# Kernel optimization log

Measured on AMD Instinct MI355X. Metric: run time of the kernel, lower is better.

Reference implementation:

```python
import jax, jax.numpy as jnp
import numpy as np

N_NODES = 50000
IN_CH = 128
HID = 128
OUT_CH = 40
N_LAYERS = 3
N_EDGES = 600000


def setup_inputs() -> dict:
    key = jax.random.key(0)
    ks = jax.random.split(key, 4 + 5 * N_LAYERS)
    x = jax.random.normal(ks[0], (N_NODES, IN_CH), dtype=jnp.float32)
    edge_attr = jax.random.normal(ks[1], (N_EDGES, 4), dtype=jnp.float32)
    edge_index = jax.random.randint(ks[2], (2, N_EDGES), 0, N_NODES, dtype=jnp.int64)
    # Per-layer MLP params ([in->hid->hid]); in==hid so stack as [L, d, d].
    def glorot(k, fan_in, fan_out):
        s = jnp.sqrt(2.0 / (fan_in + fan_out)).astype(jnp.float32)
        return jax.random.normal(k, (fan_in, fan_out), dtype=jnp.float32) * s
    W1 = jnp.stack([glorot(ks[3 + i], IN_CH if i == 0 else HID, HID) for i in range(N_LAYERS)])
    b1 = jnp.zeros((N_LAYERS, HID), dtype=jnp.float32)
    W2 = jnp.stack([glorot(ks[3 + N_LAYERS + i], HID, HID) for i in range(N_LAYERS)])
    b2 = jnp.zeros((N_LAYERS, HID), dtype=jnp.float32)
    Wc = glorot(ks[3 + 2 * N_LAYERS], HID, OUT_CH)
    bc = jnp.zeros((OUT_CH,), dtype=jnp.float32)
    return {"x": x, "edge_attr": edge_attr, "edge_index": edge_index,
            "W1": W1, "b1": b1, "W2": W2, "b2": b2, "Wc": Wc, "bc": bc}


def reference(x, edge_attr, edge_index, W1, b1, W2, b2, Wc, bc):
    # GIN node classifier, eval mode (dropout = identity, BN = identity).
    src, dst = edge_index[0], edge_index[1]
    h = x
    for i in range(N_LAYERS):
        # GINConv (eps=0): aggregate sum of neighbor features via scatter-add.
        msgs = h[src]                                   # [E, d] gather
        aggr = jax.ops.segment_sum(msgs, dst, num_segments=N_NODES)  # [N, d]
        z = h + aggr                                    # (1+eps)*x + sum
        z = jax.nn.relu(z @ W1[i] + b1[i])              # MLP hidden
        z = z @ W2[i] + b2[i]                           # MLP out
        h = jax.nn.relu(z)                              # F.relu(conv(...))
    return h @ Wc + bc                                  # [N, OUT_CH]
```

## Files before the change

### kernel.cpp

```cpp
#include <hip/hip_runtime.h>

#define N_NODES 50000
#define IN_CH 128
#define HID 128
#define OUT_CH 40
#define N_LAYERS 3
#define N_EDGES 600000
#define DSTRIDE 64
#define DEGSTRIDE 32

typedef __attribute__((ext_vector_type(8))) short short8;
typedef __attribute__((ext_vector_type(4))) float floatx4;

static __device__ __forceinline__ unsigned short f32_to_bf16(float f) {
  unsigned u = __float_as_uint(f);
  unsigned r = 0x7FFFu + ((u >> 16) & 1u);
  return (unsigned short)((u + r) >> 16);
}
static __device__ __forceinline__ float bf16_to_f32(unsigned short h) {
  return __uint_as_float(((unsigned)h) << 16);
}

#define CONV_BLOCKS 6250
#define W_BLOCKS 408
#define DEG_BLOCKS 1563

__global__ __launch_bounds__(256) void prep_all_kernel(
    const float* __restrict__ x, const float* __restrict__ W1,
    const float* __restrict__ W2, const float* __restrict__ Wc,
    unsigned short* __restrict__ xb, unsigned short* __restrict__ WT,
    unsigned short* __restrict__ WcT, unsigned short* __restrict__ hb1,
    int* __restrict__ deg) {
  const int b = blockIdx.x;
  const int t = threadIdx.x;
  if (b < CONV_BLOCKS) {
    int i = (b * 256 + t) * 4;
    if (i < N_NODES * 128) {
      float4 v = *(const float4*)(x + i);
      ushort4 o;
      o.x = f32_to_bf16(v.x); o.y = f32_to_bf16(v.y);
      o.z = f32_to_bf16(v.z); o.w = f32_to_bf16(v.w);
      *(ushort4*)(xb + i) = o;
    }
  } else if (b < CONV_BLOCKS + W_BLOCKS) {
    int o = (b - CONV_BLOCKS) * 256 + t;
    if (o < 6 * 16384) {
      int mat = o >> 14;
      int r = o & 16383;
      int n = r >> 7;
      int k = r & 127;
      const float* W = (mat < 3) ? (W1 + (size_t)mat * 16384)
                                 : (W2 + (size_t)(mat - 3) * 16384);
      WT[(size_t)mat * 16384 + (size_t)n * 128 + k] =
          f32_to_bf16(W[(size_t)k * 128 + n]);
    } else if (o < 6 * 16384 + 48 * 128) {
      int r = o - 6 * 16384;
      int n = r >> 7;
      int k = r & 127;
      float v = (n < OUT_CH) ? Wc[(size_t)k * OUT_CH + n] : 0.0f;
      WcT[(size_t)n * 128 + k] = f32_to_bf16(v);
    }
  } else if (b < CONV_BLOCKS + W_BLOCKS + DEG_BLOCKS) {
    int i = ((b - CONV_BLOCKS - W_BLOCKS) * 256 + t) * 4;
    if (i < N_NODES * DEGSTRIDE) *(int4*)(deg + i) = make_int4(0, 0, 0, 0);
  } else {
    if (t < 128) xb[(size_t)N_NODES * 128 + t] = 0;
    else hb1[(size_t)N_NODES * 128 + (t - 128)] = 0;
  }
}

#define CSR_BLOCKS 586
__global__ __launch_bounds__(256) void csr_kernel(
    const int* __restrict__ ei, int* __restrict__ deg, int* __restrict__ col) {
  int base = (blockIdx.x * 256 + threadIdx.x) * 4;
  if (base >= N_EDGES) return;
  int4 s4 = *(const int4*)(ei + base);
  int4 d4 = *(const int4*)(ei + N_EDGES + base);
  int p0 = atomicAdd(&deg[(size_t)d4.x * DEGSTRIDE], 1);
  int p1 = atomicAdd(&deg[(size_t)d4.y * DEGSTRIDE], 1);
  int p2 = atomicAdd(&deg[(size_t)d4.z * DEGSTRIDE], 1);
  int p3 = atomicAdd(&deg[(size_t)d4.w * DEGSTRIDE], 1);
  col[(size_t)d4.x * DSTRIDE + p0] = s4.x;
  col[(size_t)d4.y * DSTRIDE + p1] = s4.y;
  col[(size_t)d4.z * DSTRIDE + p2] = s4.z;
  col[(size_t)d4.w * DSTRIDE + p3] = s4.w;
}

__global__ __launch_bounds__(256) void aggregate_kernel(
    const unsigned short* __restrict__ h, const int* __restrict__ deg,
    const int* __restrict__ col, unsigned short* __restrict__ z) {
  int n = __builtin_amdgcn_readfirstlane(blockIdx.x * 4 + (threadIdx.x >> 6));
  int q = threadIdx.x & 63;
  const size_t co = (size_t)q * 2;
  ushort2 sv = *(const ushort2*)(h + (size_t)n * 128 + co);
  float ax[8], ay[8];
#pragma unroll
  for (int k = 0; k < 8; ++k) { ax[k] = 0.f; ay[k] = 0.f; }
  ax[0] = bf16_to_f32(sv.x);
  ay[0] = bf16_to_f32(sv.y);
  int dg = __builtin_amdgcn_readfirstlane(deg[(size_t)n * DEGSTRIDE]);
  int cnt = (dg + 15) & ~15;
  const int* cp = col + (size_t)n * DSTRIDE;
  for (int i = 0; i < cnt; i += 16) {
    int ss[16];
#pragma unroll
    for (int k = 0; k < 16; ++k) {
      int sl = cp[i + k];
      ss[k] = __builtin_amdgcn_readfirstlane((i + k < dg) ? sl : N_NODES);
    }
    ushort2 vv[16];
#pragma unroll
    for (int k = 0; k < 16; ++k)
      vv[k] = *(const ushort2*)(h + (size_t)ss[k] * 128 + co);
#pragma unroll
    for (int k = 0; k < 16; ++k) {
      ax[k & 7] += bf16_to_f32(vv[k].x);
      ay[k & 7] += bf16_to_f32(vv[k].y);
    }
  }
  float s0 = (ax[0] + ax[1]) + (ax[2] + ax[3]) + (ax[4] + ax[5]) + (ax[6] + ax[7]);
  float s1 = (ay[0] + ay[1]) + (ay[2] + ay[3]) + (ay[4] + ay[5]) + (ay[6] + ay[7]);
  ushort2 o;
  o.x = f32_to_bf16(s0);
  o.y = f32_to_bf16(s1);
  *(ushort2*)(z + (size_t)n * 128 + co) = o;
}

template <bool LAST>
__global__ __launch_bounds__(256) void layer_pair_kernel(
    const unsigned short* __restrict__ A, const unsigned short* __restrict__ WT1,
    const float* __restrict__ b1, const unsigned short* __restrict__ WT2,
    const float* __restrict__ b2, unsigned short* __restrict__ Z,
    const unsigned short* __restrict__ WcT, const float* __restrict__ bc,
    float* __restrict__ out, int M) {
  __shared__ __align__(16) unsigned short Wl[128][136];
  __shared__ __align__(16) unsigned short T[64][136];
  const int tid = threadIdx.x;
  const int w = tid >> 6;
  const int lane = tid & 63;
  const int qg = lane >> 4;
  const int ln = lane & 15;
  const int row0 = blockIdx.x * 64;
  const int rbase = w * 16;
  const int r0 = row0 + rbase + ln;
  const short8 zero8 = {0, 0, 0, 0, 0, 0, 0, 0};

#pragma unroll
  for (int j = 0; j < 8; ++j) {
    int slot = tid + j * 256;
    int row = slot >> 4;
    int kb = slot & 15;
    *(short8*)&Wl[row][kb * 8] = *(const short8*)(WT1 + (size_t)row * 128 + kb * 8);
  }
  __syncthreads();

  floatx4 acc[8];
#pragma unroll
  for (int ct = 0; ct < 8; ++ct) acc[ct] = (floatx4){0.f, 0.f, 0.f, 0.f};
#pragma unroll
  for (int ks = 0; ks < 4; ++ks) {
    const int koff = ks * 32 + qg * 8;
    short8 a = (r0 < M) ? *(const short8*)(A + (size_t)r0 * 128 + koff) : zero8;
#pragma unroll
    for (int ct = 0; ct < 8; ++ct) {
      short8 b = *(const short8*)&Wl[ct * 16 + ln][koff];
      acc[ct] = __builtin_amdgcn_mfma_f32_16x16x32_bf16(a, b, acc[ct], 0, 0, 0);
    }
  }
#pragma unroll
  for (int ct = 0; ct < 8; ++ct) {
    float bv = b1[ct * 16 + ln];
#pragma unroll
    for (int r = 0; r < 4; ++r) {
      float v = fmaxf(acc[ct][r] + bv, 0.0f);
      T[rbase + qg * 4 + r][ct * 16 + ln] = f32_to_bf16(v);
    }
  }

  __syncthreads();
#pragma unroll
  for (int j = 0; j < 8; ++j) {
    int slot = tid + j * 256;
    int row = slot >> 4;
    int kb = slot & 15;
    *(short8*)&Wl[row][kb * 8] = *(const short8*)(WT2 + (size_t)row * 128 + kb * 8);
  }
  __syncthreads();

  floatx4 acc2[8];
#pragma unroll
  for (int ct = 0; ct < 8; ++ct) acc2[ct] = (floatx4){0.f, 0.f, 0.f, 0.f};
#pragma unroll
  for (int ks = 0; ks < 4; ++ks) {
    const int koff = ks * 32 + qg * 8;
    short8 a = *(const short8*)&T[rbase + ln][koff];
#pragma unroll
    for (int ct = 0; ct < 8; ++ct) {
      short8 b = *(const short8*)&Wl[ct * 16 + ln][koff];
      acc2[ct] = __builtin_amdgcn_mfma_f32_16x16x32_bf16(a, b, acc2[ct], 0, 0, 0);
    }
  }
#pragma unroll
  for (int ct = 0; ct < 8; ++ct) {
    float bv = b2[ct * 16 + ln];
#pragma unroll
    for (int r = 0; r < 4; ++r) {
      float v = fmaxf(acc2[ct][r] + bv, 0.0f);
      T[rbase + qg * 4 + r][ct * 16 + ln] = f32_to_bf16(v);
    }
  }

  if (LAST) {
    floatx4 acc3[3];
#pragma unroll
    for (int ct = 0; ct < 3; ++ct) acc3[ct] = (floatx4){0.f, 0.f, 0.f, 0.f};
#pragma unroll
    for (int ks = 0; ks < 4; ++ks) {
      const int koff = ks * 32 + qg * 8;
      short8 a = *(const short8*)&T[rbase + ln][koff];
#pragma unroll
      for (int ct = 0; ct < 3; ++ct) {
        short8 b = *(const short8*)(WcT + (size_t)(ct * 16 + ln) * 128 + koff);
        acc3[ct] = __builtin_amdgcn_mfma_f32_16x16x32_bf16(a, b, acc3[ct], 0, 0, 0);
      }
    }
#pragma unroll
    for (int ct = 0; ct < 3; ++ct) {
      int colg = ct * 16 + ln;
      if (colg < OUT_CH) {
        float bv = bc[colg];
#pragma unroll
        for (int r = 0; r < 4; ++r) {
          int row = row0 + rbase + qg * 4 + r;
          if (row < M) out[(size_t)row * OUT_CH + colg] = acc3[ct][r] + bv;
        }
      }
    }
  } else {
    __syncthreads();
#pragma unroll
    for (int j = 0; j < 4; ++j) {
      int slot = tid + j * 256;
      int row = slot >> 4;
      int kb = slot & 15;
      if (row0 + row < M) {
        short8 v = *(const short8*)&T[row][kb * 8];
        *(short8*)(Z + (size_t)(row0 + row) * 128 + kb * 8) = v;
      }
    }
  }
}

extern "C" void kernel_launch(void* const* d_in, const int* in_sizes, int n_in,
                              void* d_out, int out_size, void* d_ws,
                              size_t ws_size, hipStream_t stream) {
  const float* x = (const float*)d_in[0];
  const int* ei = (const int*)d_in[2];
  const float* W1 = (const float*)d_in[3];
  const float* b1 = (const float*)d_in[4];
  const float* W2 = (const float*)d_in[5];
  const float* b2 = (const float*)d_in[6];
  const float* Wc = (const float*)d_in[7];
  const float* bc = (const float*)d_in[8];
  float* out = (float*)d_out;

  const size_t NF = (size_t)(N_NODES + 1) * 128;
  unsigned short* hb0 = (unsigned short*)d_ws;
  unsigned short* hb1 = hb0 + NF;
  unsigned short* xbf = hb1 + NF;
  unsigned short* WT = xbf + NF;
  unsigned short* WcT = WT + 6 * 16384;
  int* deg = (int*)(WcT + 48 * 128);
  int* col = deg + (size_t)N_NODES * DEGSTRIDE;

  const dim3 blk(256);
  const int aggr_grid = N_NODES / 4;
  const int pair_grid = (N_NODES + 63) / 64;

  prep_all_kernel<<<CONV_BLOCKS + W_BLOCKS + DEG_BLOCKS + 1, blk, 0, stream>>>(
      x, W1, W2, Wc, xbf, WT, WcT, hb1, deg);

  csr_kernel<<<CSR_BLOCKS, blk, 0, stream>>>(ei, deg, col);

  const unsigned short* h = xbf;
  for (int l = 0; l < N_LAYERS; ++l) {
    aggregate_kernel<<<aggr_grid, blk, 0, stream>>>(h, deg, col, hb0);
    if (l < N_LAYERS - 1) {
      layer_pair_kernel<false><<<pair_grid, blk, 0, stream>>>(
          hb0, WT + (size_t)l * 16384, b1 + (size_t)l * 128,
          WT + (size_t)(3 + l) * 16384, b2 + (size_t)l * 128, hb1,
          nullptr, nullptr, nullptr, N_NODES);
      h = hb1;
    } else {
      layer_pair_kernel<true><<<pair_grid, blk, 0, stream>>>(
          hb0, WT + (size_t)l * 16384, b1 + (size_t)l * 128,
          WT + (size_t)(3 + l) * 16384, b2 + (size_t)l * 128, nullptr,
          WcT, bc, out, N_NODES);
    }
  }
}
```

Measured before the change: 245.5 us.

## Overlap CSR build with bf16 conversion by moving deg zeroing to its own kernel

Measured after the change: 243.2 us. Within noise of the previous version (-0.9%).

```diff
diff --git a/kernel.cpp b/kernel.cpp
--- a/kernel.cpp
+++ b/kernel.cpp
@@ -7,7 +7,7 @@
 #define N_LAYERS 3
 #define N_EDGES 600000
 #define DSTRIDE 64
-#define DEGSTRIDE 32
+#define DEGSTRIDE 16
 
 typedef __attribute__((ext_vector_type(8))) short short8;
 typedef __attribute__((ext_vector_type(4))) float floatx4;
@@ -21,20 +21,41 @@
   return __uint_as_float(((unsigned)h) << 16);
 }
 
+#define ZERO_BLOCKS 782
+__global__ __launch_bounds__(256) void zero_deg_kernel(int* __restrict__ deg) {
+  int i = (blockIdx.x * 256 + threadIdx.x) * 4;
+  if (i < N_NODES * DEGSTRIDE) *(int4*)(deg + i) = make_int4(0, 0, 0, 0);
+}
+
+#define CSRB 586
 #define CONV_BLOCKS 6250
 #define W_BLOCKS 408
-#define DEG_BLOCKS 1563
-
-__global__ __launch_bounds__(256) void prep_all_kernel(
+
+__global__ __launch_bounds__(256) void prep_csr_kernel(
     const float* __restrict__ x, const float* __restrict__ W1,
     const float* __restrict__ W2, const float* __restrict__ Wc,
-    unsigned short* __restrict__ xb, unsigned short* __restrict__ WT,
-    unsigned short* __restrict__ WcT, unsigned short* __restrict__ hb1,
-    int* __restrict__ deg) {
+    const int* __restrict__ ei, unsigned short* __restrict__ xb,
+    unsigned short* __restrict__ WT, unsigned short* __restrict__ WcT,
+    unsigned short* __restrict__ hb1, int* __restrict__ deg,
+    int* __restrict__ col) {
   const int b = blockIdx.x;
   const int t = threadIdx.x;
-  if (b < CONV_BLOCKS) {
-    int i = (b * 256 + t) * 4;
+  if (b < CSRB) {
+    int base = (b * 256 + t) * 4;
+    if (base < N_EDGES) {
+      int4 s4 = *(const int4*)(ei + base);
+      int4 d4 = *(const int4*)(ei + N_EDGES + base);
+      int p0 = atomicAdd(&deg[(size_t)d4.x * DEGSTRIDE], 1);
+      int p1 = atomicAdd(&deg[(size_t)d4.y * DEGSTRIDE], 1);
+      int p2 = atomicAdd(&deg[(size_t)d4.z * DEGSTRIDE], 1);
+      int p3 = atomicAdd(&deg[(size_t)d4.w * DEGSTRIDE], 1);
+      col[(size_t)d4.x * DSTRIDE + p0] = s4.x;
+      col[(size_t)d4.y * DSTRIDE + p1] = s4.y;
+      col[(size_t)d4.z * DSTRIDE + p2] = s4.z;
+      col[(size_t)d4.w * DSTRIDE + p3] = s4.w;
+    }
+  } else if (b < CSRB + CONV_BLOCKS) {
+    int i = ((b - CSRB) * 256 + t) * 4;
     if (i < N_NODES * 128) {
       float4 v = *(const float4*)(x + i);
       ushort4 o;
@@ -42,8 +63,8 @@
       o.z = f32_to_bf16(v.z); o.w = f32_to_bf16(v.w);
       *(ushort4*)(xb + i) = o;
     }
-  } else if (b < CONV_BLOCKS + W_BLOCKS) {
-    int o = (b - CONV_BLOCKS) * 256 + t;
+  } else if (b < CSRB + CONV_BLOCKS + W_BLOCKS) {
+    int o = (b - CSRB - CONV_BLOCKS) * 256 + t;
     if (o < 6 * 16384) {
       int mat = o >> 14;
       int r = o & 16383;
@@ -60,30 +81,10 @@
       float v = (n < OUT_CH) ? Wc[(size_t)k * OUT_CH + n] : 0.0f;
       WcT[(size_t)n * 128 + k] = f32_to_bf16(v);
     }
-  } else if (b < CONV_BLOCKS + W_BLOCKS + DEG_BLOCKS) {
-    int i = ((b - CONV_BLOCKS - W_BLOCKS) * 256 + t) * 4;
-    if (i < N_NODES * DEGSTRIDE) *(int4*)(deg + i) = make_int4(0, 0, 0, 0);
   } else {
     if (t < 128) xb[(size_t)N_NODES * 128 + t] = 0;
     else hb1[(size_t)N_NODES * 128 + (t - 128)] = 0;
   }
-}
-
-#define CSR_BLOCKS 586
-__global__ __launch_bounds__(256) void csr_kernel(
-    const int* __restrict__ ei, int* __restrict__ deg, int* __restrict__ col) {
-  int base = (blockIdx.x * 256 + threadIdx.x) * 4;
-  if (base >= N_EDGES) return;
-  int4 s4 = *(const int4*)(ei + base);
-  int4 d4 = *(const int4*)(ei + N_EDGES + base);
-  int p0 = atomicAdd(&deg[(size_t)d4.x * DEGSTRIDE], 1);
-  int p1 = atomicAdd(&deg[(size_t)d4.y * DEGSTRIDE], 1);
-  int p2 = atomicAdd(&deg[(size_t)d4.z * DEGSTRIDE], 1);
-  int p3 = atomicAdd(&deg[(size_t)d4.w * DEGSTRIDE], 1);
-  col[(size_t)d4.x * DSTRIDE + p0] = s4.x;
-  col[(size_t)d4.y * DSTRIDE + p1] = s4.y;
-  col[(size_t)d4.z * DSTRIDE + p2] = s4.z;
-  col[(size_t)d4.w * DSTRIDE + p3] = s4.w;
 }
 
 __global__ __launch_bounds__(256) void aggregate_kernel(
@@ -277,10 +278,10 @@
   const int aggr_grid = N_NODES / 4;
   const int pair_grid = (N_NODES + 63) / 64;
 
-  prep_all_kernel<<<CONV_BLOCKS + W_BLOCKS + DEG_BLOCKS + 1, blk, 0, stream>>>(
-      x, W1, W2, Wc, xbf, WT, WcT, hb1, deg);
-
-  csr_kernel<<<CSR_BLOCKS, blk, 0, stream>>>(ei, deg, col);
+  zero_deg_kernel<<<ZERO_BLOCKS, blk, 0, stream>>>(deg);
+
+  prep_csr_kernel<<<CSRB + CONV_BLOCKS + W_BLOCKS + 1, blk, 0, stream>>>(
+      x, W1, W2, Wc, ei, xbf, WT, WcT, hb1, deg, col);
 
   const unsigned short* h = xbf;
   for (int l = 0; l < N_LAYERS; ++l) {
```
